# Optimization experiments

Measured on AMD Instinct MI355X. Metric: run time of the kernel, lower is better.

The kernel has to match this reference:

```python
import jax, jax.numpy as jnp
import numpy as np

N = 8192      # total packed vision tokens
D = 1280      # hidden_size
H = 16        # num_heads
K = 80        # head_dim = D // H
M = 16        # number of image segments
LMAX = 1024   # static upper bound on per-image segment length
SCALE = K ** (-0.5)
NEG = -1e30   # finite mask value (avoids NaN on fully-padded rows)


def _rotate_half(x):
    h = x.shape[-1] // 2
    return jnp.concatenate([-x[..., h:], x[..., :h]], axis=-1)


def setup_inputs() -> dict:
    key = jax.random.key(0)
    ks = jax.random.split(key, 5)
    hidden = jax.random.normal(ks[0], (N, D), jnp.float32)
    # ragged per-image lengths (sum == N, each <= LMAX)
    lengths = np.array([256, 768] * (M // 2), dtype=np.int32)
    cu = jnp.asarray(np.concatenate([[0], np.cumsum(lengths)]).astype(np.int32))
    # rotary tables, shape (N, head_dim)
    inv_freq = 1.0 / (10000.0 ** (np.arange(0, K, 2, dtype=np.float32) / K))  # (K/2,)
    freqs = np.arange(N, dtype=np.float32)[:, None] * inv_freq[None, :]       # (N, K/2)
    emb = np.concatenate([freqs, freqs], axis=-1)                              # (N, K)
    cos = jnp.asarray(np.cos(emb), jnp.float32)
    sin = jnp.asarray(np.sin(emb), jnp.float32)
    W_qkv = jax.random.normal(ks[1], (D, 3 * D), jnp.float32) * (D ** -0.5)
    b_qkv = jax.random.normal(ks[2], (3 * D,), jnp.float32) * 0.01
    W_proj = jax.random.normal(ks[3], (D, D), jnp.float32) * (D ** -0.5)
    b_proj = jax.random.normal(ks[4], (D,), jnp.float32) * 0.01
    return dict(hidden_ND=hidden, cu_seqlens=cu, cos_NK=cos, sin_NK=sin,
                W_qkv=W_qkv, b_qkv=b_qkv, W_proj=W_proj, b_proj=b_proj)


def reference(hidden_ND, cu_seqlens, cos_NK, sin_NK, W_qkv, b_qkv, W_proj, b_proj):
    n = hidden_ND.shape[0]
    # fused QKV projection
    qkv = (hidden_ND @ W_qkv + b_qkv).reshape(n, 3, H, K)
    q, k, v = qkv[:, 0], qkv[:, 1], qkv[:, 2]          # (N, H, K)
    # inline RoPE on Q/K (fp32 math, as in apply_rotary_pos_emb_vision)
    cos = cos_NK[:, None, :]
    sin = sin_NK[:, None, :]
    q = q * cos + _rotate_half(q) * sin
    k = k * cos + _rotate_half(k) * sin
    # gather packed tokens into padded per-segment blocks (honors segment sparsity:
    # no cross-segment tiles are ever materialized)
    lengths = jnp.diff(cu_seqlens)                                  # (M,)
    idx = cu_seqlens[:-1, None] + jnp.arange(LMAX)[None, :]         # (M, LMAX)
    valid = jnp.arange(LMAX)[None, :] < lengths[:, None]            # (M, LMAX)
    idxc = jnp.minimum(idx, n - 1)
    qg, kg, vg = q[idxc], k[idxc], v[idxc]                          # (M, LMAX, H, K)
    # per-segment attention
    scores = jnp.einsum('mqhd,mkhd->mhqk', qg, kg) * SCALE          # (M, H, LMAX, LMAX)
    mask = valid[:, None, :, None] & valid[:, None, None, :]
    scores = jnp.where(mask, scores, NEG)
    p = jax.nn.softmax(scores, axis=-1)
    og = jnp.einsum('mhqk,mkhd->mqhd', p, vg)                       # (M, LMAX, H, K)
    # scatter back to packed layout: token n -> (segment, position)
    seg = jnp.searchsorted(cu_seqlens[1:], jnp.arange(n), side='right')
    pos = jnp.arange(n) - cu_seqlens[seg]
    attn_ND = og[seg, pos].reshape(n, H * K)
    return attn_ND @ W_proj + b_proj
```

## Files before the change

### kernel.cpp

```cpp
#include <hip/hip_runtime.h>
#include <hip/hip_bf16.h>
#include <stdint.h>

#define NTOK 8192
#define DMODEL 1280
#define NHEAD 16
#define HDIM 80
#define NSEG 16
#define SCALE_F 0.11180339887498949f
#define NEG_F -1e30f

typedef __bf16 bf16x8 __attribute__((ext_vector_type(8)));
typedef float f32x4 __attribute__((ext_vector_type(4)));

__device__ __forceinline__ void gload_lds16(const void* g, void* l) {
  __builtin_amdgcn_global_load_lds((__attribute__((address_space(1))) void*)g,
                                   (__attribute__((address_space(3))) void*)l,
                                   16, 0, 0);
}

__global__ __launch_bounds__(256)
void cvt_f32_to_bf16(const float* __restrict__ src, __hip_bfloat16* __restrict__ dst) {
  int i = (blockIdx.x * 256 + threadIdx.x) * 4;
  float4 v = *(const float4*)(src + i);
  __align__(8) __hip_bfloat16 o[4] = {__float2bfloat16(v.x), __float2bfloat16(v.y),
                                      __float2bfloat16(v.z), __float2bfloat16(v.w)};
  *(uint2*)(dst + i) = *(const uint2*)o;
}

__global__ __launch_bounds__(256)
void transpose_w(const float* __restrict__ src, __hip_bfloat16* __restrict__ dst,
                 int R, int C) {
  __shared__ __hip_bfloat16 tile[32][33];
  int c0 = blockIdx.x * 32, r0 = blockIdx.y * 32;
  int tx = threadIdx.x & 31, ty = threadIdx.x >> 5;
#pragma unroll
  for (int i = 0; i < 4; ++i) {
    int r = ty + i * 8;
    tile[r][tx] = __float2bfloat16(src[(size_t)(r0 + r) * C + c0 + tx]);
  }
  __syncthreads();
#pragma unroll
  for (int i = 0; i < 4; ++i) {
    int r = ty + i * 8;
    dst[(size_t)(c0 + r) * R + r0 + tx] = tile[tx][r];
  }
}

__global__ __launch_bounds__(256)
void rope2(__hip_bfloat16* __restrict__ qkv,
           const float* __restrict__ cosb, const float* __restrict__ sinb) {
  int t = blockIdx.x * 256 + threadIdx.x;
  int p = t % 5;
  int rest = t / 5;
  int h = rest & 15;
  int qk = (rest >> 4) & 1;
  int n = rest >> 5;
  size_t base = (size_t)n * 3840 + qk * 1280 + h * 80 + p * 8;
  const float* cb = cosb + n * 80 + p * 8;
  const float* sb = sinb + n * 80 + p * 8;
  float4 cA = *(const float4*)cb, cB = *(const float4*)(cb + 4);
  float4 cC = *(const float4*)(cb + 40), cD = *(const float4*)(cb + 44);
  float4 sA = *(const float4*)sb, sB = *(const float4*)(sb + 4);
  float4 sC = *(const float4*)(sb + 40), sD = *(const float4*)(sb + 44);
  float c0[8] = {cA.x, cA.y, cA.z, cA.w, cB.x, cB.y, cB.z, cB.w};
  float c1[8] = {cC.x, cC.y, cC.z, cC.w, cD.x, cD.y, cD.z, cD.w};
  float s0[8] = {sA.x, sA.y, sA.z, sA.w, sB.x, sB.y, sB.z, sB.w};
  float s1[8] = {sC.x, sC.y, sC.z, sC.w, sD.x, sD.y, sD.z, sD.w};
  uint4 lou = *(const uint4*)(qkv + base);
  uint4 hiu = *(const uint4*)(qkv + base + 40);
  __align__(16) __hip_bfloat16 lo[8], hh[8], olo[8], ohi[8];
  *(uint4*)lo = lou; *(uint4*)hh = hiu;
#pragma unroll
  for (int e = 0; e < 8; ++e) {
    float x0 = __bfloat162float(lo[e]);
    float x1 = __bfloat162float(hh[e]);
    olo[e] = __float2bfloat16(x0 * c0[e] - x1 * s0[e]);
    ohi[e] = __float2bfloat16(x1 * c1[e] + x0 * s1[e]);
  }
  *(uint4*)(qkv + base) = *(const uint4*)olo;
  *(uint4*)(qkv + base + 40) = *(const uint4*)ohi;
}

template <bool OUT_F32, bool A_F32>
__global__ __launch_bounds__(256)
void gemm128(const void* __restrict__ Av, int lda,
             const __hip_bfloat16* __restrict__ Bt,
             const float* __restrict__ bias,
             void* __restrict__ Cv, int M, int N, int K) {
  __shared__ __align__(16) __hip_bfloat16 lds[8192];
  const int tid = threadIdx.x;
  const int lane = tid & 63;
  const int wave = tid >> 6;
  const int wr = wave >> 1, wc = wave & 1;
  const int lr = lane & 15;
  const int lk = (lane >> 4) << 3;
  const int m0 = blockIdx.x * 128;
  const int n0 = blockIdx.y * 128;

  f32x4 zero = {0.f, 0.f, 0.f, 0.f};
  f32x4 acc[4][4];
#pragma unroll
  for (int i = 0; i < 4; ++i)
#pragma unroll
    for (int j = 0; j < 4; ++j) acc[i][j] = zero;

  for (int k0 = 0; k0 < K; k0 += 32) {
#pragma unroll
    for (int j = 0; j < 2; ++j) {
      int v = j * 256 + tid;
      int row = v >> 2;
      int cb = (v & 3) << 3;
      gload_lds16(Bt + (size_t)(n0 + row) * K + k0 + cb,
                  &lds[4096 + wave * 512 + j * 2048]);
    }
    if constexpr (A_F32) {
      const float* A32 = (const float*)Av;
      float4 vv[4];
#pragma unroll
      for (int j = 0; j < 4; ++j) {
        int task = j * 256 + tid;
        int row = task >> 3, cc = task & 7;
        vv[j] = *(const float4*)(A32 + (size_t)(m0 + row) * lda + k0 + cc * 4);
      }
#pragma unroll
      for (int j = 0; j < 4; ++j) {
        int task = j * 256 + tid;
        int row = task >> 3, cc = task & 7;
        __align__(8) __hip_bfloat16 t[4] = {
            __float2bfloat16(vv[j].x), __float2bfloat16(vv[j].y),
            __float2bfloat16(vv[j].z), __float2bfloat16(vv[j].w)};
        *(uint2*)&lds[row * 32 + cc * 4] = *(const uint2*)t;
      }
    } else {
      const __hip_bfloat16* Abf = (const __hip_bfloat16*)Av;
#pragma unroll
      for (int j = 0; j < 2; ++j) {
        int v = j * 256 + tid;
        int row = v >> 2;
        int cb = (v & 3) << 3;
        gload_lds16(Abf + (size_t)(m0 + row) * lda + k0 + cb,
                    &lds[wave * 512 + j * 2048]);
      }
    }
    __syncthreads();

    bf16x8 af[4], bfr[4];
#pragma unroll
    for (int i = 0; i < 4; ++i) {
      af[i]  = *(const bf16x8*)&lds[(wr * 64 + i * 16 + lr) * 32 + lk];
      bfr[i] = *(const bf16x8*)&lds[4096 + (wc * 64 + i * 16 + lr) * 32 + lk];
    }
#pragma unroll
    for (int i = 0; i < 4; ++i)
#pragma unroll
      for (int j = 0; j < 4; ++j)
        acc[i][j] = __builtin_amdgcn_mfma_f32_16x16x32_bf16(af[i], bfr[j], acc[i][j], 0, 0, 0);
    __syncthreads();
  }

  const int r0 = (lane >> 4) << 2;
#pragma unroll
  for (int j = 0; j < 4; ++j) {
    int col = n0 + wc * 64 + j * 16 + lr;
    float bv = bias[col];
#pragma unroll
    for (int i = 0; i < 4; ++i) {
      int rowb = m0 + wr * 64 + i * 16 + r0;
#pragma unroll
      for (int r = 0; r < 4; ++r) {
        float val = acc[i][j][r] + bv;
        if (OUT_F32)
          ((float*)Cv)[(size_t)(rowb + r) * N + col] = val;
        else
          ((__hip_bfloat16*)Cv)[(size_t)(rowb + r) * N + col] = __float2bfloat16(val);
      }
    }
  }
}

__global__ __launch_bounds__(256, 3)
void attn_fwd(__hip_bfloat16* __restrict__ qkv, const int* __restrict__ cu) {
  const int bid = blockIdx.x;
  const int l = (bid & 7) * 288 + (bid >> 3);
  const int h = l / 144;
  const int pid = l - h * 144;
  int seg = -1, qt = 0, start = 0, L = 0;
  int accq = 0;
#pragma unroll 1
  for (int s2 = 0; s2 < NSEG; ++s2) {
    int st = cu[s2], en = cu[s2 + 1];
    int len = en - st;
    int nq = (len + 63) >> 6;
    if (seg < 0 && pid < accq + nq) { seg = s2; qt = pid - accq; start = st; L = len; }
    accq += nq;
  }
  if (seg < 0) return;

  __shared__ __align__(16) __hip_bfloat16 Ks[2][64 * 80];
  __shared__ __align__(16) __hip_bfloat16 Vs[2][80 * 72];
  __shared__ __align__(16) __hip_bfloat16 Ps[4][16 * 72];

  const int tid = threadIdx.x;
  const int lane = tid & 63;
  const int wave = tid >> 6;
  const int lr = lane & 15;
  const int hi = lane >> 4;
  const int lk = hi * 8;
  const int nt = (L + 63) >> 6;

  bf16x8 aq[3];
  {
    bf16x8 z;
#pragma unroll
    for (int e = 0; e < 8; ++e) z[e] = (__bf16)0.0f;
    int qr = qt * 64 + wave * 16 + lr;
    if (qr > L - 1) qr = L - 1;
    const __hip_bfloat16* qp = qkv + (size_t)(start + qr) * 3840 + h * 80;
    bf16x8 a0 = *(const bf16x8*)(qp + lk);
    bf16x8 a1 = *(const bf16x8*)(qp + 32 + lk);
    bf16x8 a2 = (hi < 2) ? *(const bf16x8*)(qp + 64 + lk) : z;
#pragma unroll
    for (int e = 0; e < 8; ++e) {
      a0[e] = (__bf16)((float)a0[e] * SCALE_F);
      a1[e] = (__bf16)((float)a1[e] * SCALE_F);
      a2[e] = (__bf16)((float)a2[e] * SCALE_F);
    }
    aq[0] = a0; aq[1] = a1; aq[2] = a2;
  }

  const __hip_bfloat16* kbase = qkv + (size_t)start * 3840 + 1280 + h * 80;
  const __hip_bfloat16* vbase = qkv + (size_t)start * 3840 + 2560 + h * 80;

  auto stageK = [&](int t, int buf) {
#pragma unroll
    for (int j = 0; j < 3; ++j) {
      int i = wave + 4 * j;
      if (i < 10) {
        int E = i * 512 + lane * 8;
        int r = E / 80;
        int c = E - r * 80;
        int g = t * 64 + r;
        if (g > L - 1) g = L - 1;
        gload_lds16(kbase + (size_t)g * 3840 + c, (char*)&Ks[buf][0] + i * 1024);
      }
    }
  };
  uint4 vr[3];
  auto loadV = [&](int t) {
    int g = t * 64 + lane;
    if (g > L - 1) g = L - 1;
    size_t roff = (size_t)g * 3840;
#pragma unroll
    for (int j = 0; j < 3; ++j) {
      int c = wave + 4 * j;
      if (c < 10) vr[j] = *(const uint4*)(vbase + roff + c * 8);
    }
  };
  auto writeV = [&](int buf) {
#pragma unroll
    for (int j = 0; j < 3; ++j) {
      int c = wave + 4 * j;
      if (c < 10) {
        __align__(16) __hip_bfloat16 tmp[8];
        *(uint4*)tmp = vr[j];
#pragma unroll
        for (int e = 0; e < 8; ++e) Vs[buf][(c * 8 + e) * 72 + lane] = tmp[e];
      }
    }
  };

  float m_run[4], l_part[4];
  f32x4 fz = {0.f, 0.f, 0.f, 0.f};
  f32x4 accO[5];
#pragma unroll
  for (int r = 0; r < 4; ++r) { m_run[r] = NEG_F; l_part[r] = 0.f; }
#pragma unroll
  for (int d = 0; d < 5; ++d) accO[d] = fz;

  stageK(0, 0);
  loadV(0);
  writeV(0);
  loadV(nt > 1 ? 1 : 0);
  __syncthreads();

  int cur = 0;
  for (int t = 0; t < nt; ++t) {
    const bool more = (t + 1 < nt);
    if (more) {
      stageK(t + 1, cur ^ 1);
      writeV(cur ^ 1);
      loadV(t + 2 < nt ? t + 2 : nt - 1);
    }

    f32x4 s[4] = {fz, fz, fz, fz};
#pragma unroll
    for (int ks = 0; ks < 3; ++ks) {
#pragma unroll
      for (int j = 0; j < 4; ++j) {
        bf16x8 bk = *(const bf16x8*)&Ks[cur][(j * 16 + lr) * 80 + ks * 32 + lk];
        s[j] = __builtin_amdgcn_mfma_f32_16x16x32_bf16(aq[ks], bk, s[j], 0, 0, 0);
      }
    }
    if (t * 64 + 64 > L) {
#pragma unroll
      for (int j = 0; j < 4; ++j) {
        bool vj = (t * 64 + j * 16 + lr) < L;
#pragma unroll
        for (int r = 0; r < 4; ++r)
          s[j][r] = vj ? s[j][r] : NEG_F;
      }
    }
    float mx[4];
    bool need = false;
#pragma unroll
    for (int r = 0; r < 4; ++r) {
      mx[r] = fmaxf(fmaxf(s[0][r], s[1][r]), fmaxf(s[2][r], s[3][r]));
      need |= mx[r] > m_run[r] + 8.0f;
    }
    if (__any(need)) {
#pragma unroll
      for (int off = 1; off < 16; off <<= 1)
#pragma unroll
        for (int r = 0; r < 4; ++r)
          mx[r] = fmaxf(mx[r], __shfl_xor(mx[r], off, 64));
#pragma unroll
      for (int r = 0; r < 4; ++r) {
        float mn = fmaxf(m_run[r], mx[r]);
        float sf = __expf(m_run[r] - mn);
        m_run[r] = mn;
        l_part[r] *= sf;
#pragma unroll
        for (int d = 0; d < 5; ++d) accO[d][r] *= sf;
      }
    }
#pragma unroll
    for (int r = 0; r < 4; ++r) {
      float a0 = __expf(s[0][r] - m_run[r]); s[0][r] = a0;
      float a1 = __expf(s[1][r] - m_run[r]); s[1][r] = a1;
      float a2 = __expf(s[2][r] - m_run[r]); s[2][r] = a2;
      float a3 = __expf(s[3][r] - m_run[r]); s[3][r] = a3;
      l_part[r] += (a0 + a1) + (a2 + a3);
    }

    __hip_bfloat16* pw = &Ps[wave][0];
#pragma unroll
    for (int j = 0; j < 4; ++j)
#pragma unroll
      for (int r = 0; r < 4; ++r)
        pw[(hi * 4 + r) * 72 + j * 16 + lr] = __float2bfloat16(s[j][r]);
    asm volatile("s_waitcnt lgkmcnt(0)" ::: "memory");
    __builtin_amdgcn_sched_barrier(0);
    bf16x8 ap0 = *(const bf16x8*)&pw[lr * 72 + lk];
    bf16x8 ap1 = *(const bf16x8*)&pw[lr * 72 + 32 + lk];
#pragma unroll
    for (int d = 0; d < 5; ++d) {
      bf16x8 bv0 = *(const bf16x8*)&Vs[cur][(d * 16 + lr) * 72 + lk];
      bf16x8 bv1 = *(const bf16x8*)&Vs[cur][(d * 16 + lr) * 72 + 32 + lk];
      accO[d] = __builtin_amdgcn_mfma_f32_16x16x32_bf16(ap0, bv0, accO[d], 0, 0, 0);
      accO[d] = __builtin_amdgcn_mfma_f32_16x16x32_bf16(ap1, bv1, accO[d], 0, 0, 0);
    }

    __syncthreads();
    cur ^= 1;
  }

#pragma unroll
  for (int off = 1; off < 16; off <<= 1)
#pragma unroll
    for (int r = 0; r < 4; ++r)
      l_part[r] += __shfl_xor(l_part[r], off, 64);
  float rl[4];
#pragma unroll
  for (int r = 0; r < 4; ++r) rl[r] = 1.0f / l_part[r];
#pragma unroll
  for (int d = 0; d < 5; ++d)
#pragma unroll
    for (int r = 0; r < 4; ++r) {
      int row = qt * 64 + wave * 16 + hi * 4 + r;
      if (row < L)
        qkv[(size_t)(start + row) * 3840 + h * 80 + d * 16 + lr] =
            __float2bfloat16(accO[d][r] * rl[r]);
    }
}

extern "C" void kernel_launch(void* const* d_in, const int* in_sizes, int n_in,
                              void* d_out, int out_size, void* d_ws, size_t ws_size,
                              hipStream_t stream) {
  const float* hidden = (const float*)d_in[0];
  const int*   cu     = (const int*)d_in[1];
  const float* cosb   = (const float*)d_in[2];
  const float* sinb   = (const float*)d_in[3];
  const float* Wqkv   = (const float*)d_in[4];
  const float* bqkv   = (const float*)d_in[5];
  const float* Wproj  = (const float*)d_in[6];
  const float* bproj  = (const float*)d_in[7];
  float* out = (float*)d_out;
  char* ws = (char*)d_ws;

  __hip_bfloat16* qkv    = (__hip_bfloat16*)(ws);
  __hip_bfloat16* wqkvT  = (__hip_bfloat16*)(ws + 62914560);
  __hip_bfloat16* wprojT = (__hip_bfloat16*)(ws + 72744960);
  __hip_bfloat16* hbf    = (__hip_bfloat16*)(ws + 76021760);
  const bool use_hbf = ws_size >= (size_t)96993280;

  transpose_w<<<dim3(120, 40), 256, 0, stream>>>(Wqkv, wqkvT, 1280, 3840);
  transpose_w<<<dim3(40, 40), 256, 0, stream>>>(Wproj, wprojT, 1280, 1280);
  if (use_hbf) {
    cvt_f32_to_bf16<<<10240, 256, 0, stream>>>(hidden, hbf);
    gemm128<false, false><<<dim3(64, 30), 256, 0, stream>>>(hbf, 1280, wqkvT, bqkv, qkv, 8192, 3840, 1280);
  } else {
    gemm128<false, true><<<dim3(64, 30), 256, 0, stream>>>(hidden, 1280, wqkvT, bqkv, qkv, 8192, 3840, 1280);
  }
  rope2<<<5120, 256, 0, stream>>>(qkv, cosb, sinb);
  attn_fwd<<<2304, 256, 0, stream>>>(qkv, cu);
  gemm128<true, false><<<dim3(64, 10), 256, 0, stream>>>(qkv, 3840, wprojT, bproj, out, 8192, 1280, 1280);
}
```

Measured before the change: 279.3 us.

## Add 256x256-tile triple-buffered GEMM for QKV projection

```diff
diff --git a/kernel.cpp b/kernel.cpp
--- a/kernel.cpp
+++ b/kernel.cpp
@@ -179,6 +179,111 @@
   }
 }
 
+__global__ __launch_bounds__(512, 2)
+void gemm256(const __hip_bfloat16* __restrict__ A,
+             const __hip_bfloat16* __restrict__ Bt,
+             const float* __restrict__ bias,
+             __hip_bfloat16* __restrict__ C, int M, int N, int K) {
+  __shared__ __align__(16) __hip_bfloat16 lds[49152];
+  const int tid = threadIdx.x;
+  const int lane = tid & 63;
+  const int wave = tid >> 6;
+  const int wr = wave >> 2;
+  const int wc = wave & 3;
+  const int lr = lane & 15;
+  const int hi = lane >> 4;
+  const int m0 = blockIdx.x * 256;
+  const int n0 = blockIdx.y * 256;
+
+  const __hip_bfloat16* srcA = A + (size_t)(m0 + (tid >> 2)) * K + (tid & 3) * 8;
+  const __hip_bfloat16* srcB = Bt + (size_t)(n0 + (tid >> 2)) * K + (tid & 3) * 8;
+  const size_t row128 = (size_t)128 * K;
+
+  auto stageA = [&](int kt, int b) {
+    const __hip_bfloat16* s = srcA + kt * 32;
+    gload_lds16(s,          &lds[b * 16384 + tid * 8]);
+    gload_lds16(s + row128, &lds[b * 16384 + 4096 + tid * 8]);
+  };
+  auto stageB = [&](int kt, int b) {
+    const __hip_bfloat16* s = srcB + kt * 32;
+    gload_lds16(s,          &lds[b * 16384 + 8192 + tid * 8]);
+    gload_lds16(s + row128, &lds[b * 16384 + 8192 + 4096 + tid * 8]);
+  };
+
+  f32x4 acc[8][4];
+  f32x4 fz = {0.f, 0.f, 0.f, 0.f};
+#pragma unroll
+  for (int i = 0; i < 8; ++i)
+#pragma unroll
+    for (int j = 0; j < 4; ++j) acc[i][j] = fz;
+
+  const int nkt = K >> 5;
+  stageA(0, 0); stageB(0, 0);
+  stageA(1, 1); stageB(1, 1);
+  asm volatile("s_waitcnt vmcnt(4)" ::: "memory");
+  __builtin_amdgcn_sched_barrier(0);
+  __builtin_amdgcn_s_barrier();
+
+  for (int t = 0; t < nkt; ++t) {
+    const int b = t % 3;
+    const int bs = (t + 2) % 3;
+    const int ktn = (t + 2 < nkt) ? t + 2 : nkt - 1;
+    const __hip_bfloat16* Ab = &lds[b * 16384 + (wr * 128) * 32];
+    const __hip_bfloat16* Bb = &lds[b * 16384 + 8192 + (wc * 64) * 32];
+
+    bf16x8 bf[4], af[4];
+#pragma unroll
+    for (int j = 0; j < 4; ++j) bf[j] = *(const bf16x8*)&Bb[(j * 16 + lr) * 32 + hi * 8];
+#pragma unroll
+    for (int i = 0; i < 4; ++i) af[i] = *(const bf16x8*)&Ab[(i * 16 + lr) * 32 + hi * 8];
+    stageA(ktn, bs);
+    __builtin_amdgcn_sched_barrier(0);
+    __builtin_amdgcn_s_barrier();
+    asm volatile("s_waitcnt lgkmcnt(0)" ::: "memory");
+    __builtin_amdgcn_sched_barrier(0);
+    __builtin_amdgcn_s_setprio(1);
+#pragma unroll
+    for (int i = 0; i < 4; ++i)
+#pragma unroll
+      for (int j = 0; j < 4; ++j)
+        acc[i][j] = __builtin_amdgcn_mfma_f32_16x16x32_bf16(af[i], bf[j], acc[i][j], 0, 0, 0);
+    __builtin_amdgcn_s_setprio(0);
+    __builtin_amdgcn_sched_barrier(0);
+    __builtin_amdgcn_s_barrier();
+
+#pragma unroll
+    for (int i = 0; i < 4; ++i) af[i] = *(const bf16x8*)&Ab[((i + 4) * 16 + lr) * 32 + hi * 8];
+    stageB(ktn, bs);
+    asm volatile("s_waitcnt vmcnt(4)" ::: "memory");
+    __builtin_amdgcn_sched_barrier(0);
+    __builtin_amdgcn_s_barrier();
+    asm volatile("s_waitcnt lgkmcnt(0)" ::: "memory");
+    __builtin_amdgcn_sched_barrier(0);
+    __builtin_amdgcn_s_setprio(1);
+#pragma unroll
+    for (int i = 0; i < 4; ++i)
+#pragma unroll
+      for (int j = 0; j < 4; ++j)
+        acc[4 + i][j] = __builtin_amdgcn_mfma_f32_16x16x32_bf16(af[i], bf[j], acc[4 + i][j], 0, 0, 0);
+    __builtin_amdgcn_s_setprio(0);
+    __builtin_amdgcn_sched_barrier(0);
+    __builtin_amdgcn_s_barrier();
+  }
+
+#pragma unroll
+  for (int j = 0; j < 4; ++j) {
+    int col = n0 + wc * 64 + j * 16 + lr;
+    float bv = bias[col];
+#pragma unroll
+    for (int i = 0; i < 8; ++i) {
+      int row0 = m0 + wr * 128 + i * 16 + hi * 4;
+#pragma unroll
+      for (int r = 0; r < 4; ++r)
+        C[(size_t)(row0 + r) * N + col] = __float2bfloat16(acc[i][j][r] + bv);
+    }
+  }
+}
+
 __global__ __launch_bounds__(256, 3)
 void attn_fwd(__hip_bfloat16* __restrict__ qkv, const int* __restrict__ cu) {
   const int bid = blockIdx.x;
@@ -408,7 +513,7 @@
   transpose_w<<<dim3(40, 40), 256, 0, stream>>>(Wproj, wprojT, 1280, 1280);
   if (use_hbf) {
     cvt_f32_to_bf16<<<10240, 256, 0, stream>>>(hidden, hbf);
-    gemm128<false, false><<<dim3(64, 30), 256, 0, stream>>>(hbf, 1280, wqkvT, bqkv, qkv, 8192, 3840, 1280);
+    gemm256<<<dim3(32, 15), 512, 0, stream>>>(hbf, wqkvT, bqkv, qkv, 8192, 3840, 1280);
   } else {
     gemm128<false, true><<<dim3(64, 30), 256, 0, stream>>>(hidden, 1280, wqkvT, bqkv, qkv, 8192, 3840, 1280);
   }
```

Measured after the change: 257.8 us. 7.7% less time.
